# Optimization experiments

Hardware: AMD Instinct MI355X
Metric: run time of the kernel (lower is better)

Reference implementation:

```python
import jax, jax.numpy as jnp
import numpy as np

CLASSES = 21
IOU_THRESH = 0.5
ALPHA = 0.25   # focal loss alpha
GAMMA = 2.0    # focal loss gamma
SL1_BETA = 1.0 # torch SmoothL1Loss default beta
CLS_W = 1.0
REG_W = 1.0
NUM_ANCHORS = 98304
NUM_TARGETS = 1024


def _compute_iou(boxes_a, boxes_b):
    # boxes_a: [T,4], boxes_b: [A,4] in (x1,y1,x2,y2) -> [T,A]
    lt = jnp.maximum(boxes_a[:, None, :2], boxes_b[None, :, :2])
    rb = jnp.minimum(boxes_a[:, None, 2:], boxes_b[None, :, 2:])
    wh = jnp.clip(rb - lt, 0.0)
    inter = wh[..., 0] * wh[..., 1]
    area_a = (boxes_a[:, 2] - boxes_a[:, 0]) * (boxes_a[:, 3] - boxes_a[:, 1])
    area_b = (boxes_b[:, 2] - boxes_b[:, 0]) * (boxes_b[:, 3] - boxes_b[:, 1])
    union = area_a[:, None] + area_b[None, :] - inter
    return inter / jnp.maximum(union, 1e-8)


def _encode(boxes, anchors):
    bw = boxes[:, 2] - boxes[:, 0]
    bh = boxes[:, 3] - boxes[:, 1]
    bcx = boxes[:, 0] + 0.5 * bw
    bcy = boxes[:, 1] + 0.5 * bh
    aw = anchors[:, 2] - anchors[:, 0]
    ah = anchors[:, 3] - anchors[:, 1]
    acx = anchors[:, 0] + 0.5 * aw
    acy = anchors[:, 1] + 0.5 * ah
    tx = (bcx - acx) / aw
    ty = (bcy - acy) / ah
    tw = jnp.log(jnp.maximum(bw, 1e-8) / aw)
    th = jnp.log(jnp.maximum(bh, 1e-8) / ah)
    return jnp.stack([tx, ty, tw, th], axis=1)


def _focal_loss(logits, targets):
    # elementwise sigmoid focal loss (no reduction)
    p = jax.nn.sigmoid(logits)
    # numerically stable BCE with logits
    ce = jnp.maximum(logits, 0.0) - logits * targets + jnp.log1p(jnp.exp(-jnp.abs(logits)))
    p_t = p * targets + (1.0 - p) * (1.0 - targets)
    alpha_t = ALPHA * targets + (1.0 - ALPHA) * (1.0 - targets)
    return alpha_t * (1.0 - p_t) ** GAMMA * ce


def _smooth_l1(diff):
    ad = jnp.abs(diff)
    return jnp.where(ad < SL1_BETA, 0.5 * diff * diff / SL1_BETA, ad - 0.5 * SL1_BETA)


def setup_inputs() -> dict:
    key = jax.random.key(0)
    kA, kW, kT, kJ, kL, kC, kB = jax.random.split(key, 7)
    A, T = NUM_ANCHORS, NUM_TARGETS
    centers = jax.random.uniform(kA, (A, 2), minval=0.15, maxval=0.85)
    sizes = jax.random.uniform(kW, (A, 2), minval=0.05, maxval=0.30)
    anchors = jnp.concatenate([centers - 0.5 * sizes, centers + 0.5 * sizes], axis=1)
    # targets = jittered anchors so IoU >= 0.5 matches exist
    idx = jax.random.randint(kT, (T,), 0, A)
    jitter = jax.random.uniform(kJ, (T, 4), minval=-0.01, maxval=0.01)
    target_boxes = anchors[idx] + jitter
    target_labels = jax.random.randint(kL, (T,), 0, CLASSES)
    classification_preds = jax.random.normal(kC, (A, CLASSES), dtype=jnp.float32)
    boxes_preds = jax.random.normal(kB, (A, 4), dtype=jnp.float32)
    return {
        'classification_preds': classification_preds,
        'boxes_preds': boxes_preds,
        'anchors': anchors,
        'target_boxes': target_boxes,
        'target_labels': target_labels,
    }


def reference(classification_preds, boxes_preds, anchors, target_boxes, target_labels):
    iou = _compute_iou(target_boxes, anchors)  # [T, A]

    # anchor-side matching -> classification targets
    max_iou_for_anchors = jnp.max(iou, axis=0)          # [A]
    target_ids_for_anchors = jnp.argmax(iou, axis=0)     # [A]
    positive_mask = max_iou_for_anchors >= IOU_THRESH    # [A] bool
    n_pos = jnp.sum(positive_mask.astype(jnp.float32))
    onehot = jax.nn.one_hot(target_labels[target_ids_for_anchors], CLASSES, dtype=jnp.float32)
    cls_targets = jnp.where(positive_mask[:, None], onehot, 0.0)
    cls_loss = jnp.sum(_focal_loss(classification_preds, cls_targets)) / n_pos

    max_iou_for_targets = jnp.max(iou, axis=1)          # [T]
    anchor_ids_for_targets = jnp.argmax(iou, axis=1)     # [T]
    t_mask = (max_iou_for_targets >= IOU_THRESH).astype(jnp.float32)  # [T]
    matched_anchors = anchors[anchor_ids_for_targets]    # [T,4]
    encoded = _encode(target_boxes, matched_anchors)     # [T,4]
    pred = boxes_preds[anchor_ids_for_targets]           # [T,4]
    diff = (pred - encoded) * t_mask[:, None]
    n_match = jnp.maximum(jnp.sum(t_mask), 1.0)
    reg_loss = jnp.sum(_smooth_l1(diff)) / (n_match * 4.0)  # mean over matched elements

    w_cls = cls_loss * CLS_W
    w_reg = reg_loss * REG_W
    return (w_cls + w_reg, w_cls, w_reg)
```

## Files before the change

### kernel.cpp

```cpp
#include <hip/hip_runtime.h>
#include <stdint.h>

#define NA 98304
#define NT 1024
#define NC 21
#define NBLK 1536
#define HI_MIN 0xBF000000u
#define C3S 0.33333f


__device__ __forceinline__ float f0(float x) {
    const float ax = fabsf(x);
    const float u  = __expf(-ax);
    const float ce = fmaxf(x, 0.f) + __logf(1.f + u);
    const float p  = (x >= 0.f ? 1.f : u) / (1.f + u);
    return 0.75f * p * p * ce;
}
__device__ __forceinline__ float f1(float x) {
    const float ax = fabsf(x);
    const float u  = __expf(-ax);
    const float ce = fmaxf(x, 0.f) - x + __logf(1.f + u);
    const float p  = (x >= 0.f ? 1.f : u) / (1.f + u);
    const float q  = 1.f - p;
    return 0.25f * q * q * ce;
}
__device__ __forceinline__ unsigned long long mk_key(float iou, unsigned int idx) {
    return ((unsigned long long)(__float_as_uint(iou) | 0x80000000u) << 32) |
           (unsigned long long)(0xFFFFFFFFu - idx);
}
__device__ __forceinline__ float smooth_l1(float d) {
    const float ad = fabsf(d);
    return (ad < 1.f) ? 0.5f * d * d : ad - 0.5f;
}
__device__ __forceinline__ unsigned long long aload64(const unsigned long long* p) {
    return __hip_atomic_load(p, __ATOMIC_RELAXED, __HIP_MEMORY_SCOPE_AGENT);
}
__device__ __forceinline__ float aloadf(const float* p) {
    return __hip_atomic_load(p, __ATOMIC_RELAXED, __HIP_MEMORY_SCOPE_AGENT);
}
__device__ __forceinline__ int aloadi(const int* p) {
    return __hip_atomic_load(p, __ATOMIC_RELAXED, __HIP_MEMORY_SCOPE_AGENT);
}

#define SCREEN(j, m)                                                        \
    {                                                                       \
        const float w0 = fminf(az4[j], tb.z) + fminf(negax[j], tb.x);       \
        const float w  = fmaxf(w0, 0.f);                                    \
        const float h0 = fminf(aw4[j], tb.w) + fminf(negay[j], tb.y);       \
        m |= (fmaf(w, h0, -ar34[j]) >= sac) ? (1ull << i) : 0ull;           \
    }

#define WALK(j, mj, bk)                                                     \
    if (mj != 0ull) {                                                       \
        unsigned long long m = mj;                                          \
        do {                                                                \
            const int i = __ffsll(m) - 1;                                   \
            m &= m - 1;                                                     \
            const int t = tb0 + 4 * i;                                      \
            const float4 tb = s_t[t];                                       \
            const float sa = (tb.z + tb.x) * (tb.w + tb.y);                 \
            const float arj = (az4[j] + negax[j]) * (aw4[j] + negay[j]);    \
            const float w = fmaxf(fminf(az4[j], tb.z) + fminf(negax[j], tb.x), 0.f); \
            const float h = fmaxf(fminf(aw4[j], tb.w) + fminf(negay[j], tb.y), 0.f); \
            const float inter = w * h;                                      \
            const float uni   = (arj + sa) - inter;                         \
            const float iou   = inter / uni;                                \
            const unsigned long long ak = mk_key(iou, (unsigned int)t);     \
            if (ak > bk) bk = ak;                                           \
            atomicMax(&s_tk[t], mk_key(iou, (unsigned int)(abase + j)));    \
        } while (m != 0ull);                                                \
    }

#define FOLD(bk)                                                            \
    {                                                                       \
        unsigned long long o_ = __shfl_xor(bk, 16);                         \
        if (o_ > bk) bk = o_;                                               \
        o_ = __shfl_xor(bk, 32);                                            \
        if (o_ > bk) bk = o_;                                               \
    }

__global__ __launch_bounds__(256, 6) void k_all(
    const float* __restrict__ preds,
    const float4* __restrict__ preds4,
    const int* __restrict__ tlabels,
    const float4* __restrict__ anchors,
    const float4* __restrict__ tboxes,
    const float4* __restrict__ bpreds,
    unsigned long long* __restrict__ tkeys,
    float* __restrict__ part,
    int* __restrict__ npos_part,
    int* __restrict__ done_g,
    int* __restrict__ done2,
    float* __restrict__ out)
{
    __shared__ float4 s_t[NT];
    __shared__ unsigned long long s_tk[NT];
    __shared__ unsigned long long s_bk[4][64];
    __shared__ float  s_f[4];
    __shared__ int    s_fin;
    __shared__ double s_d[4];
    __shared__ int    s_i[4];
    __shared__ float  s_s[4], s_m[4];

    const int tid  = threadIdx.x;
    const int b    = blockIdx.x;
    const int lane = tid & 63, wid = tid >> 6;

    float4 tbl[4];
    #pragma unroll
    for (int k = 0; k < 4; ++k) tbl[k] = tboxes[tid + 256 * k];

    float facc;
    {
        const int pb = b * 336;
        const float4 v0 = preds4[pb + tid];
        facc = (f0(v0.x) + f0(v0.y)) + (f0(v0.z) + f0(v0.w));
        if (tid < 80) {
            const float4 v1 = preds4[pb + 256 + tid];
            facc += (f0(v1.x) + f0(v1.y)) + (f0(v1.z) + f0(v1.w));
        }
    }

    #pragma unroll
    for (int k = 0; k < 4; ++k) {
        s_t[tid + 256 * k]  = make_float4(-tbl[k].x, -tbl[k].y, tbl[k].z, tbl[k].w);
        s_tk[tid + 256 * k] = 0ull;
    }

    const int qd    = lane & 15;
    const int sl    = lane >> 4;
    const int abase = b * 64 + 4 * qd;
    float negax[4], negay[4], az4[4], aw4[4], ar34[4];
    #pragma unroll
    for (int j = 0; j < 4; ++j) {
        const float4 A = anchors[abase + j];
        negax[j] = -A.x; negay[j] = -A.y;
        az4[j]   = A.z;  aw4[j]   = A.w;
        ar34[j]  = ((A.z - A.x) * (A.w - A.y)) * C3S;
    }
    __syncthreads();

    unsigned long long m0 = 0ull, m1 = 0ull, m2 = 0ull, m3 = 0ull;
    const int tb0 = wid * 256 + sl;
    #pragma unroll 8
    for (int i = 0; i < 64; ++i) {
        const float4 tb = s_t[tb0 + 4 * i];
        const float sa  = (tb.z + tb.x) * (tb.w + tb.y);
        const float sac = sa * C3S;
        SCREEN(0, m0)
        SCREEN(1, m1)
        SCREEN(2, m2)
        SCREEN(3, m3)
    }

    unsigned long long bk0 = 0ull, bk1 = 0ull, bk2 = 0ull, bk3 = 0ull;
    WALK(0, m0, bk0)
    WALK(1, m1, bk1)
    WALK(2, m2, bk2)
    WALK(3, m3, bk3)

    FOLD(bk0) FOLD(bk1) FOLD(bk2) FOLD(bk3)
    if (sl == 0) {
        s_bk[wid][4 * qd + 0] = bk0;
        s_bk[wid][4 * qd + 1] = bk1;
        s_bk[wid][4 * qd + 2] = bk2;
        s_bk[wid][4 * qd + 3] = bk3;
    }

    for (int o = 32; o > 0; o >>= 1) facc += __shfl_down(facc, o);
    if (lane == 0) s_f[wid] = facc;
    __syncthreads();

    #pragma unroll
    for (int k = 0; k < 4; ++k) {
        const int t = tid + 256 * k;
        const unsigned long long v = s_tk[t];
        if (v != 0ull) atomicMax(&tkeys[t], v);
    }

    float corrv = 0.f;
    int   cnt   = 0;
    if (tid < 64) {
        unsigned long long k0 = s_bk[0][tid];
        const unsigned long long k1 = s_bk[1][tid];
        const unsigned long long k2 = s_bk[2][tid];
        const unsigned long long k3 = s_bk[3][tid];
        if (k1 > k0) k0 = k1;
        if (k2 > k0) k0 = k2;
        if (k3 > k0) k0 = k3;
        if ((unsigned int)(k0 >> 32) >= HI_MIN) {
            cnt = 1;
            const int tI  = (int)(0xFFFFFFFFu - (unsigned int)k0);
            const int lab = tlabels[tI];
            const float x = preds[(b * 64 + tid) * NC + lab];
            corrv = f1(x) - f0(x);
        }
        for (int o = 32; o > 0; o >>= 1) {
            corrv += __shfl_down(corrv, o);
            cnt   += __shfl_down(cnt, o);
        }
    }
    if (tid == 0) {
        __hip_atomic_store(&part[b], (s_f[0] + s_f[1] + s_f[2] + s_f[3]) + corrv,
                           __ATOMIC_RELAXED, __HIP_MEMORY_SCOPE_AGENT);
        __hip_atomic_store(&npos_part[b], cnt,
                           __ATOMIC_RELAXED, __HIP_MEMORY_SCOPE_AGENT);
    }
    __syncthreads();
    if (tid == 0) {
        __threadfence();
        int fin = 0;
        if (atomicAdd(&done_g[b & 63], 1) == 23) {
            __threadfence();
            fin = (atomicAdd(done2, 1) == 63);
        }
        s_fin = fin;
    }
    __syncthreads();
    if (!s_fin) return;
    __builtin_amdgcn_fence(__ATOMIC_ACQUIRE, "agent");

    double cl = 0.0;
    int    np = 0;
    #pragma unroll
    for (int j = 0; j < 6; ++j) {
        const int i = tid + 256 * j;
        cl += (double)aloadf(&part[i]);
        np += aloadi(&npos_part[i]);
    }
    float s = 0.f, m = 0.f;
    #pragma unroll
    for (int j = 0; j < 4; ++j) {
        const int t = tid + 256 * j;
        const unsigned long long key = aload64(&tkeys[t]);
        if ((unsigned int)(key >> 32) >= HI_MIN) {
            const unsigned int ga = 0xFFFFFFFFu - (unsigned int)key;
            const float4 tb  = tboxes[t];
            const float4 abx = anchors[ga];
            const float4 pb  = bpreds[ga];
            const float bw = tb.z - tb.x, bh = tb.w - tb.y;
            const float bcx = tb.x + 0.5f * bw, bcy = tb.y + 0.5f * bh;
            const float aw = abx.z - abx.x, ah = abx.w - abx.y;
            const float acx = abx.x + 0.5f * aw, acy = abx.y + 0.5f * ah;
            const float tx = (bcx - acx) / aw;
            const float ty = (bcy - acy) / ah;
            const float tw = logf(fmaxf(bw, 1e-8f) / aw);
            const float th = logf(fmaxf(bh, 1e-8f) / ah);
            s += smooth_l1(pb.x - tx) + smooth_l1(pb.y - ty) +
                 smooth_l1(pb.z - tw) + smooth_l1(pb.w - th);
            m += 1.f;
        }
    }
    for (int o = 32; o > 0; o >>= 1) {
        cl += __shfl_down(cl, o);
        np += __shfl_down(np, o);
        s  += __shfl_down(s, o);
        m  += __shfl_down(m, o);
    }
    __syncthreads();
    if (lane == 0) { s_d[wid] = cl; s_i[wid] = np; s_s[wid] = s; s_m[wid] = m; }
    __syncthreads();
    if (tid == 0) {
        const double cls_sum = s_d[0] + s_d[1] + s_d[2] + s_d[3];
        const int    npos    = s_i[0] + s_i[1] + s_i[2] + s_i[3];
        const float  rs      = s_s[0] + s_s[1] + s_s[2] + s_s[3];
        const float  rm      = s_m[0] + s_m[1] + s_m[2] + s_m[3];
        const float cls = (float)(cls_sum / (double)npos);
        const float reg = rs / (fmaxf(rm, 1.f) * 4.f);
        out[0] = cls + reg;
        out[1] = cls;
        out[2] = reg;
    }
}

extern "C" void kernel_launch(void* const* d_in, const int* in_sizes, int n_in,
                              void* d_out, int out_size, void* d_ws, size_t ws_size,
                              hipStream_t stream) {
    const float*  preds   = (const float*)d_in[0];
    const float4* preds4  = (const float4*)d_in[0];
    const float4* bpreds  = (const float4*)d_in[1];
    const float4* anchors = (const float4*)d_in[2];
    const float4* tboxes  = (const float4*)d_in[3];
    const int*    tlabels = (const int*)d_in[4];

    char* ws = (char*)d_ws;
    int*    done2     = (int*)(ws + 0);
    int*    done_g    = (int*)(ws + 128);
    float*  part      = (float*)(ws + 1024);
    int*    npos_part = (int*)(ws + 8192);
    unsigned long long* tkeys = (unsigned long long*)(ws + 16384);

    hipMemsetAsync(d_ws, 0, 1024, stream);

    k_all<<<dim3(NBLK), 256, 0, stream>>>(
        preds, preds4, tlabels, anchors, tboxes, bpreds,
        tkeys, part, npos_part, done_g, done2, (float*)d_out);
}
```

Measured before the change: 127.5 us.

## Screen anchor-target IoU candidates with packed fp16 math, exact fp32 recheck

Replaces the fp32 IoU>=0.5 screening loop with packed half-precision (v_pk_*_f16) arithmetic that tests two targets per instruction. Boxes are rounded upward and the threshold constant is loosened slightly so the screen stays conservative. Candidates are then rechecked exactly in fp32, reading target boxes from global memory instead of shared. This halves the ALU work and shared-memory loads in the screening loop, at the cost of rounding conversions, more false-positive candidates, and global loads inside the walk.

```diff
diff --git a/kernel.cpp b/kernel.cpp
--- a/kernel.cpp
+++ b/kernel.cpp
@@ -6,7 +6,10 @@
 #define NC 21
 #define NBLK 1536
 #define HI_MIN 0xBF000000u
-#define C3S 0.33333f
+#define C3SH 0.332f
+
+typedef unsigned int u32;
+typedef unsigned long long u64;
 
 
 __device__ __forceinline__ float f0(float x) {
@@ -24,15 +27,15 @@
     const float q  = 1.f - p;
     return 0.25f * q * q * ce;
 }
-__device__ __forceinline__ unsigned long long mk_key(float iou, unsigned int idx) {
-    return ((unsigned long long)(__float_as_uint(iou) | 0x80000000u) << 32) |
-           (unsigned long long)(0xFFFFFFFFu - idx);
+__device__ __forceinline__ u64 mk_key(float iou, u32 idx) {
+    return ((u64)(__float_as_uint(iou) | 0x80000000u) << 32) |
+           (u64)(0xFFFFFFFFu - idx);
 }
 __device__ __forceinline__ float smooth_l1(float d) {
     const float ad = fabsf(d);
     return (ad < 1.f) ? 0.5f * d * d : ad - 0.5f;
 }
-__device__ __forceinline__ unsigned long long aload64(const unsigned long long* p) {
+__device__ __forceinline__ u64 aload64(const u64* p) {
     return __hip_atomic_load(p, __ATOMIC_RELAXED, __HIP_MEMORY_SCOPE_AGENT);
 }
 __device__ __forceinline__ float aloadf(const float* p) {
@@ -42,38 +45,67 @@
     return __hip_atomic_load(p, __ATOMIC_RELAXED, __HIP_MEMORY_SCOPE_AGENT);
 }
 
-#define SCREEN(j, m)                                                        \
+__device__ __forceinline__ unsigned short ru16(float x) {
+    _Float16 h = (_Float16)x;
+    const float b = (float)h;
+    unsigned short u = __builtin_bit_cast(unsigned short, h);
+    if (b < x) u = (u & 0x8000u) ? (unsigned short)(u - 1) : (unsigned short)(u + 1);
+    return u;
+}
+__device__ __forceinline__ u32 dup16(unsigned short h) {
+    return (u32)h | ((u32)h << 16);
+}
+
+__device__ __forceinline__ u32 pk_min(u32 a, u32 b) {
+    u32 d; asm("v_pk_min_f16 %0, %1, %2" : "=v"(d) : "v"(a), "v"(b)); return d;
+}
+__device__ __forceinline__ u32 pk_max(u32 a, u32 b) {
+    u32 d; asm("v_pk_max_f16 %0, %1, %2" : "=v"(d) : "v"(a), "v"(b)); return d;
+}
+__device__ __forceinline__ u32 pk_add(u32 a, u32 b) {
+    u32 d; asm("v_pk_add_f16 %0, %1, %2" : "=v"(d) : "v"(a), "v"(b)); return d;
+}
+__device__ __forceinline__ u32 pk_fma(u32 a, u32 b, u32 c) {
+    u32 d; asm("v_pk_fma_f16 %0, %1, %2, %3" : "=v"(d) : "v"(a), "v"(b), "v"(c)); return d;
+}
+
+#define SCREEN16(j, m)                                                      \
     {                                                                       \
-        const float w0 = fminf(az4[j], tb.z) + fminf(negax[j], tb.x);       \
-        const float w  = fmaxf(w0, 0.f);                                    \
-        const float h0 = fminf(aw4[j], tb.w) + fminf(negay[j], tb.y);       \
-        m |= (fmaf(w, h0, -ar34[j]) >= sac) ? (1ull << i) : 0ull;           \
+        const u32 w0 = pk_add(pk_min(azh[j], tz2), pk_min(naxh[j], ntx2)); \
+        const u32 w  = pk_max(w0, 0u);                                      \
+        const u32 h0 = pk_add(pk_min(awh[j], tw2), pk_min(nayh[j], nty2)); \
+        const u32 nr = pk_add(narch[j], nsac2);                             \
+        const u32 d  = pk_fma(w, h0, nr);                                   \
+        const u32 s  = ~d & 0x80008000u;                                    \
+        m |= (u64)((s >> 15) & 1u) << (2 * i);                              \
+        m |= (u64)((s >> 31) & 1u) << (2 * i + 1);                          \
     }
 
 #define WALK(j, mj, bk)                                                     \
     if (mj != 0ull) {                                                       \
-        unsigned long long m = mj;                                          \
+        u64 m = mj;                                                         \
+        const float4 A  = anchors[abase + j];                               \
+        const float  ar = (A.z - A.x) * (A.w - A.y);                        \
         do {                                                                \
-            const int i = __ffsll(m) - 1;                                   \
+            const int bpos = __ffsll(m) - 1;                                \
             m &= m - 1;                                                     \
-            const int t = tb0 + 4 * i;                                      \
-            const float4 tb = s_t[t];                                       \
-            const float sa = (tb.z + tb.x) * (tb.w + tb.y);                 \
-            const float arj = (az4[j] + negax[j]) * (aw4[j] + negay[j]);    \
-            const float w = fmaxf(fminf(az4[j], tb.z) + fminf(negax[j], tb.x), 0.f); \
-            const float h = fmaxf(fminf(aw4[j], tb.w) + fminf(negay[j], tb.y), 0.f); \
+            const int t = wid * 256 + 2 * sl + 8 * (bpos >> 1) + (bpos & 1);\
+            const float4 tb = tboxes[t];                                    \
+            const float sa = (tb.z - tb.x) * (tb.w - tb.y);                 \
+            const float w = fmaxf(fminf(A.z, tb.z) - fmaxf(A.x, tb.x), 0.f);\
+            const float h = fmaxf(fminf(A.w, tb.w) - fmaxf(A.y, tb.y), 0.f);\
             const float inter = w * h;                                      \
-            const float uni   = (arj + sa) - inter;                         \
+            const float uni   = (ar + sa) - inter;                          \
             const float iou   = inter / uni;                                \
-            const unsigned long long ak = mk_key(iou, (unsigned int)t);     \
+            const u64 ak = mk_key(iou, (u32)t);                             \
             if (ak > bk) bk = ak;                                           \
-            atomicMax(&s_tk[t], mk_key(iou, (unsigned int)(abase + j)));    \
+            atomicMax(&s_tk[t], mk_key(iou, (u32)(abase + j)));             \
         } while (m != 0ull);                                                \
     }
 
 #define FOLD(bk)                                                            \
     {                                                                       \
-        unsigned long long o_ = __shfl_xor(bk, 16);                         \
+        u64 o_ = __shfl_xor(bk, 16);                                        \
         if (o_ > bk) bk = o_;                                               \
         o_ = __shfl_xor(bk, 32);                                            \
         if (o_ > bk) bk = o_;                                               \
@@ -86,16 +118,16 @@
     const float4* __restrict__ anchors,
     const float4* __restrict__ tboxes,
     const float4* __restrict__ bpreds,
-    unsigned long long* __restrict__ tkeys,
+    u64* __restrict__ tkeys,
     float* __restrict__ part,
     int* __restrict__ npos_part,
     int* __restrict__ done_g,
     int* __restrict__ done2,
     float* __restrict__ out)
 {
-    __shared__ float4 s_t[NT];
-    __shared__ unsigned long long s_tk[NT];
-    __shared__ unsigned long long s_bk[4][64];
+    __shared__ u32 s_tp[512 * 8];
+    __shared__ u64 s_tk[NT];
+    __shared__ u64 s_bk[4][64];
     __shared__ float  s_f[4];
     __shared__ int    s_fin;
     __shared__ double s_d[4];
@@ -106,9 +138,10 @@
     const int b    = blockIdx.x;
     const int lane = tid & 63, wid = tid >> 6;
 
-    float4 tbl[4];
-    #pragma unroll
-    for (int k = 0; k < 4; ++k) tbl[k] = tboxes[tid + 256 * k];
+    const float4 t0a = tboxes[2 * tid];
+    const float4 t0b = tboxes[2 * tid + 1];
+    const float4 t1a = tboxes[2 * tid + 512];
+    const float4 t1b = tboxes[2 * tid + 513];
 
     float facc;
     {
@@ -121,39 +154,56 @@
         }
     }
 
-    #pragma unroll
-    for (int k = 0; k < 4; ++k) {
-        s_t[tid + 256 * k]  = make_float4(-tbl[k].x, -tbl[k].y, tbl[k].z, tbl[k].w);
-        s_tk[tid + 256 * k] = 0ull;
+    {
+        #pragma unroll
+        for (int pp = 0; pp < 2; ++pp) {
+            const float4 ta = pp ? t1a : t0a;
+            const float4 tb = pp ? t1b : t0b;
+            const int p = tid + 256 * pp;
+            const u32 tz2  = (u32)ru16(ta.z)  | ((u32)ru16(tb.z)  << 16);
+            const u32 ntx2 = (u32)ru16(-ta.x) | ((u32)ru16(-tb.x) << 16);
+            const u32 tw2  = (u32)ru16(ta.w)  | ((u32)ru16(tb.w)  << 16);
+            const u32 nty2 = (u32)ru16(-ta.y) | ((u32)ru16(-tb.y) << 16);
+            const float qa = ((ta.z - ta.x) * (ta.w - ta.y)) * C3SH;
+            const float qb = ((tb.z - tb.x) * (tb.w - tb.y)) * C3SH;
+            const u32 nsac2 = (u32)ru16(-qa) | ((u32)ru16(-qb) << 16);
+            uint4* dst = reinterpret_cast<uint4*>(&s_tp[p * 8]);
+            *dst = make_uint4(tz2, ntx2, tw2, nty2);
+            s_tp[p * 8 + 4] = nsac2;
+        }
+        #pragma unroll
+        for (int k = 0; k < 4; ++k) s_tk[tid + 256 * k] = 0ull;
     }
 
     const int qd    = lane & 15;
     const int sl    = lane >> 4;
     const int abase = b * 64 + 4 * qd;
-    float negax[4], negay[4], az4[4], aw4[4], ar34[4];
+    u32 azh[4], naxh[4], awh[4], nayh[4], narch[4];
     #pragma unroll
     for (int j = 0; j < 4; ++j) {
         const float4 A = anchors[abase + j];
-        negax[j] = -A.x; negay[j] = -A.y;
-        az4[j]   = A.z;  aw4[j]   = A.w;
-        ar34[j]  = ((A.z - A.x) * (A.w - A.y)) * C3S;
-    }
-    __syncthreads();
-
-    unsigned long long m0 = 0ull, m1 = 0ull, m2 = 0ull, m3 = 0ull;
-    const int tb0 = wid * 256 + sl;
-    #pragma unroll 8
-    for (int i = 0; i < 64; ++i) {
-        const float4 tb = s_t[tb0 + 4 * i];
-        const float sa  = (tb.z + tb.x) * (tb.w + tb.y);
-        const float sac = sa * C3S;
-        SCREEN(0, m0)
-        SCREEN(1, m1)
-        SCREEN(2, m2)
-        SCREEN(3, m3)
-    }
-
-    unsigned long long bk0 = 0ull, bk1 = 0ull, bk2 = 0ull, bk3 = 0ull;
+        azh[j]   = dup16(ru16(A.z));
+        naxh[j]  = dup16(ru16(-A.x));
+        awh[j]   = dup16(ru16(A.w));
+        nayh[j]  = dup16(ru16(-A.y));
+        narch[j] = dup16(ru16(-((A.z - A.x) * (A.w - A.y)) * C3SH));
+    }
+    __syncthreads();
+
+    u64 m0 = 0ull, m1 = 0ull, m2 = 0ull, m3 = 0ull;
+    const int qb0 = (wid * 128 + sl) * 8;
+    #pragma unroll
+    for (int i = 0; i < 32; ++i) {
+        const uint4 c = *reinterpret_cast<const uint4*>(&s_tp[qb0 + 32 * i]);
+        const u32 tz2 = c.x, ntx2 = c.y, tw2 = c.z, nty2 = c.w;
+        const u32 nsac2 = s_tp[qb0 + 32 * i + 4];
+        SCREEN16(0, m0)
+        SCREEN16(1, m1)
+        SCREEN16(2, m2)
+        SCREEN16(3, m3)
+    }
+
+    u64 bk0 = 0ull, bk1 = 0ull, bk2 = 0ull, bk3 = 0ull;
     WALK(0, m0, bk0)
     WALK(1, m1, bk1)
     WALK(2, m2, bk2)
@@ -174,23 +224,23 @@
     #pragma unroll
     for (int k = 0; k < 4; ++k) {
         const int t = tid + 256 * k;
-        const unsigned long long v = s_tk[t];
+        const u64 v = s_tk[t];
         if (v != 0ull) atomicMax(&tkeys[t], v);
     }
 
     float corrv = 0.f;
     int   cnt   = 0;
     if (tid < 64) {
-        unsigned long long k0 = s_bk[0][tid];
-        const unsigned long long k1 = s_bk[1][tid];
-        const unsigned long long k2 = s_bk[2][tid];
-        const unsigned long long k3 = s_bk[3][tid];
+        u64 k0 = s_bk[0][tid];
+        const u64 k1 = s_bk[1][tid];
+        const u64 k2 = s_bk[2][tid];
+        const u64 k3 = s_bk[3][tid];
         if (k1 > k0) k0 = k1;
         if (k2 > k0) k0 = k2;
         if (k3 > k0) k0 = k3;
-        if ((unsigned int)(k0 >> 32) >= HI_MIN) {
+        if ((u32)(k0 >> 32) >= HI_MIN) {
             cnt = 1;
-            const int tI  = (int)(0xFFFFFFFFu - (unsigned int)k0);
+            const int tI  = (int)(0xFFFFFFFFu - (u32)k0);
             const int lab = tlabels[tI];
             const float x = preds[(b * 64 + tid) * NC + lab];
             corrv = f1(x) - f0(x);
@@ -232,9 +282,9 @@
     #pragma unroll
     for (int j = 0; j < 4; ++j) {
         const int t = tid + 256 * j;
-        const unsigned long long key = aload64(&tkeys[t]);
-        if ((unsigned int)(key >> 32) >= HI_MIN) {
-            const unsigned int ga = 0xFFFFFFFFu - (unsigned int)key;
+        const u64 key = aload64(&tkeys[t]);
+        if ((u32)(key >> 32) >= HI_MIN) {
+            const u32 ga = 0xFFFFFFFFu - (u32)key;
             const float4 tb  = tboxes[t];
             const float4 abx = anchors[ga];
             const float4 pb  = bpreds[ga];
@@ -284,11 +334,11 @@
     const int*    tlabels = (const int*)d_in[4];
 
     char* ws = (char*)d_ws;
-    int*    done2     = (int*)(ws + 0);
-    int*    done_g    = (int*)(ws + 128);
-    float*  part      = (float*)(ws + 1024);
-    int*    npos_part = (int*)(ws + 8192);
-    unsigned long long* tkeys = (unsigned long long*)(ws + 16384);
+    int*  done2     = (int*)(ws + 0);
+    int*  done_g    = (int*)(ws + 128);
+    float* part     = (float*)(ws + 1024);
+    int*  npos_part = (int*)(ws + 8192);
+    u64*  tkeys     = (u64*)(ws + 16384);
 
     hipMemsetAsync(d_ws, 0, 1024, stream);
 
```

New measurement: 162.8 us. 27.7% more time.
